# Optimization experiments

Measured on AMD Instinct MI355X. Metric: run time of the kernel, lower is better.

The kernel has to match this reference:

```python
import jax, jax.numpy as jnp
import numpy as np

B, N, F_IN, DIM, TOPK = 64, 1024, 10, 64, 20
EPS = 1e-5  # BatchNorm eps
NEG_SLOPE = 0.2


def _bn_eval(x, gamma, beta, mean, var):
    # eval-mode BatchNorm1d over the channel (last) axis
    return (x - mean) * jax.lax.rsqrt(var + EPS) * gamma + beta


def setup_inputs() -> dict:
    key = jax.random.key(0)
    ks = jax.random.split(key, 10)
    return {
        "data": jax.random.normal(ks[0], (B, N, F_IN), jnp.float32),
        "emb": jax.random.normal(ks[1], (N, DIM), jnp.float32),
        "W_lin": jax.random.normal(ks[2], (F_IN, DIM), jnp.float32),
        "att_i": jax.random.normal(ks[3], (DIM,), jnp.float32),
        "att_j": jax.random.normal(ks[4], (DIM,), jnp.float32),
        "att_em_i": jax.random.normal(ks[5], (DIM,), jnp.float32),
        "att_em_j": jax.random.normal(ks[6], (DIM,), jnp.float32),
        "gnn_bias": jax.random.normal(ks[7], (DIM,), jnp.float32),
        "bn1_gamma": jnp.ones((DIM,), jnp.float32),
        "bn1_beta": jnp.zeros((DIM,), jnp.float32),
        "bn1_mean": jnp.zeros((DIM,), jnp.float32),
        "bn1_var": jnp.ones((DIM,), jnp.float32),
        "bn2_gamma": jnp.ones((DIM,), jnp.float32),
        "bn2_beta": jnp.zeros((DIM,), jnp.float32),
        "bn2_mean": jnp.zeros((DIM,), jnp.float32),
        "bn2_var": jnp.ones((DIM,), jnp.float32),
        "out_W": jax.random.normal(ks[8], (DIM, 1), jnp.float32),
        "out_b": jax.random.normal(ks[9], (1,), jnp.float32),
    }


def reference(data, emb, W_lin, att_i, att_j, att_em_i, att_em_j, gnn_bias,
              bn1_gamma, bn1_beta, bn1_mean, bn1_var,
              bn2_gamma, bn2_beta, bn2_mean, bn2_var, out_W, out_b):
    Bn, Nn, _ = data.shape
    BN_nodes = Bn * Nn
    x = data.reshape(BN_nodes, -1)                      # [B*N, F_IN] (input is detached in torch)

    # ---- dynamic graph: cosine similarity of (detached) node embeddings, top-k per row ----
    w = jax.lax.stop_gradient(emb)                      # weights_arr = embedding.detach()
    norms = jnp.linalg.norm(w, axis=-1)                 # [N]
    cos = (w @ w.T) / (norms[:, None] * norms[None, :])  # [N, N]
    topk_idx = jax.lax.top_k(cos, TOPK)[1]              # [N, K], gated_j (message sources)
    src = topk_idx.reshape(-1)                          # j
    dst = jnp.repeat(jnp.arange(Nn), TOPK)              # i
    offs = (jnp.arange(Bn) * Nn)[:, None]               # per-graph node offsets
    bsrc = (src[None, :] + offs).reshape(-1)            # [B*N*K]
    bdst = (dst[None, :] + offs).reshape(-1)
    self_mask = bsrc == bdst                            # edges killed by remove_self_loops
    loops = jnp.arange(BN_nodes)                        # add_self_loops
    e_src = jnp.concatenate([bsrc, loops])              # [E]
    e_dst = jnp.concatenate([bdst, loops])
    e_mask = jnp.concatenate([self_mask, jnp.zeros(BN_nodes, bool)])

    # ---- GAT-style attention message passing (heads=1, concat=False, aggr='add') ----
    h = x @ W_lin                                       # [B*N, DIM]
    h_i, h_j = h[e_dst], h[e_src]                       # gathers, [E, DIM]
    emb_i = emb[e_dst % Nn]                             # embedding repeated per batch graph
    emb_j = emb[e_src % Nn]
    logit = (h_i * att_i).sum(-1) + (emb_i * att_em_i).sum(-1) \
          + (h_j * att_j).sum(-1) + (emb_j * att_em_j).sum(-1)  # [E]
    logit = jnp.where(logit > 0, logit, NEG_SLOPE * logit)       # leaky_relu(0.2)
    logit = jnp.where(e_mask, -1e30, logit)             # removed self-loops get zero weight
    seg_max = jax.ops.segment_max(logit, e_dst, num_segments=BN_nodes)
    ex = jnp.where(e_mask, 0.0, jnp.exp(logit - seg_max[e_dst]))
    seg_sum = jax.ops.segment_sum(ex, e_dst, num_segments=BN_nodes)
    alpha = ex / seg_sum[e_dst]                         # segment softmax over incoming edges
    agg = jax.ops.segment_sum(h_j * alpha[:, None], e_dst, num_segments=BN_nodes)
    agg = agg + gnn_bias                                # [B*N, DIM]
    gcn = jax.nn.relu(_bn_eval(agg, bn1_gamma, bn1_beta, bn1_mean, bn1_var))

    # ---- output head: multiply by node embedding, BN+ReLU, Linear(DIM->1) ----
    y = gcn.reshape(Bn, Nn, DIM) * emb[None, :, :]
    y = jax.nn.relu(_bn_eval(y, bn2_gamma, bn2_beta, bn2_mean, bn2_var))
    out = y @ out_W + out_b                             # [B, N, 1]; dropout is inference no-op
    return out.reshape(Bn, Nn)
```

## Files before the change

kernel.cpp:

```cpp
#include <hip/hip_runtime.h>
#include <hip/hip_bf16.h>

#define N_NODES 1024
#define B_SZ 64
#define F_IN 10
#define DIM 64
#define TOPK 20
#define BN_TOT (B_SZ * N_NODES)

#define GT_BLKS 256
#define HS_BLKS 4096
#define AB_BLKS (GT_BLKS + 1 + HS_BLKS)

__global__ __launch_bounds__(256) void k_build(
    const float* __restrict__ data, const float* __restrict__ emb,
    const float* __restrict__ W_lin,
    const float* __restrict__ att_i, const float* __restrict__ att_j,
    const float* __restrict__ att_em_i, const float* __restrict__ att_em_j,
    const float* __restrict__ gnn_bias,
    const float* __restrict__ g1, const float* __restrict__ b1,
    const float* __restrict__ m1, const float* __restrict__ v1,
    const float* __restrict__ g2, const float* __restrict__ b2,
    const float* __restrict__ m2, const float* __restrict__ v2,
    __hip_bfloat16* __restrict__ h, float* __restrict__ ddt,
    float* __restrict__ sst, int* __restrict__ tk, float4* __restrict__ bnp) {
    const int bid = blockIdx.x;
    const int t = threadIdx.x;
    const int lane = t & 63, w = t >> 6;

    if (bid < GT_BLKS) {
        __shared__ float As[4][64];
        __shared__ float P[64][65];
        const int r0 = bid * 4;
        As[t >> 6][t & 63] = emb[(r0 + (t >> 6)) * DIM + (t & 63)];
        __syncthreads();
        float av = As[w][lane];
        float nni = av * av;
#pragma unroll
        for (int m = 32; m >= 1; m >>= 1) nni += __shfl_xor(nni, m, 64);
        const float ni = sqrtf(nni);
        float v[16];
        for (int p = 0; p < 16; ++p) {
            __syncthreads();
#pragma unroll
            for (int k = 0; k < 16; ++k) {
                int idx = t + k * 256;
                P[idx >> 6][idx & 63] = emb[(p * 64 + (idx >> 6)) * DIM + (idx & 63)];
            }
            __syncthreads();
            float dot = 0.f, nsq = 0.f;
#pragma unroll
            for (int d = 0; d < 64; ++d) {
                float pv = P[lane][d];
                dot = fmaf(As[w][d], pv, dot);
                nsq = fmaf(pv, pv, nsq);
            }
            v[p] = dot / (ni * sqrtf(nsq));
        }
        int* tkr = tk + (r0 + w) * TOPK;
        for (int it = 0; it < TOPK; ++it) {
            float bv = v[0];
            int bp = 0;
#pragma unroll
            for (int p = 1; p < 16; ++p)
                if (v[p] > bv) { bv = v[p]; bp = p; }
            int bidx = lane + bp * 64;
#pragma unroll
            for (int m = 32; m >= 1; m >>= 1) {
                float ov = __shfl_xor(bv, m, 64);
                int oi = __shfl_xor(bidx, m, 64);
                if (ov > bv || (ov == bv && oi < bidx)) { bv = ov; bidx = oi; }
            }
            if (lane == 0) tkr[it] = bidx;
            if ((bidx & 63) == lane) v[bidx >> 6] = -3.0e38f;
        }
        return;
    }

    if (bid == GT_BLKS) {
        if (t < DIM) {
            float a1 = g1[t] * rsqrtf(v1[t] + 1e-5f);
            float c1 = (gnn_bias[t] - m1[t]) * a1 + b1[t];
            float a2 = g2[t] * rsqrtf(v2[t] + 1e-5f);
            float c2 = b2[t] - m2[t] * a2;
            bnp[t] = make_float4(a1, c1, a2, c2);
        }
        return;
    }

    {
        const int base = (bid - GT_BLKS - 1) * 16 + w * 4;
        float wl[F_IN];
#pragma unroll
        for (int f = 0; f < F_IN; ++f) wl[f] = W_lin[f * DIM + lane];
        const float ai = att_i[lane], aj = att_j[lane];
        const float aei = att_em_i[lane], aej = att_em_j[lane];
#pragma unroll
        for (int r = 0; r < 4; ++r) {
            const int node = base + r;
            const int i = node & (N_NODES - 1);
            const float ev = emb[i * DIM + lane];
            const float* dp = data + node * F_IN;
            float hv = 0.f;
#pragma unroll
            for (int f = 0; f < F_IN; ++f) hv = fmaf(dp[f], wl[f], hv);
            h[node * DIM + lane] = __float2bfloat16(hv);
            float s1 = fmaf(hv, ai, ev * aei);
            float s2 = fmaf(hv, aj, ev * aej);
#pragma unroll
            for (int m = 32; m >= 1; m >>= 1) {
                s1 += __shfl_xor(s1, m, 64);
                s2 += __shfl_xor(s2, m, 64);
            }
            if (lane == 0) { ddt[node] = s1; sst[node] = s2; }
        }
    }
}

__global__ __launch_bounds__(256) void k_main(
    const __hip_bfloat16* __restrict__ h, const float* __restrict__ emb,
    const float* __restrict__ ddt, const float* __restrict__ sst,
    const int* __restrict__ tk, const float4* __restrict__ bnp,
    const float* __restrict__ outW, const float* __restrict__ outB,
    float* __restrict__ out) {
    const int bid = blockIdx.x;
    const int nb = (bid & 7) * 2048 + (bid >> 3);
    const int w = threadIdx.x >> 6, lane = threadIdx.x & 63;
    const int node = nb * 4 + w;
    const int i = node & (N_NODES - 1);
    const int bbase = node & ~(N_NODES - 1);

    int j = i;
    if (lane < TOPK) j = tk[i * TOPK + lane];

    float sv = 0.f;
    if (lane <= TOPK) sv = sst[bbase + j];
    const float ddv = ddt[node];

    const __hip_bfloat16* hb = h + (size_t)bbase * DIM + lane;
    float hvf[TOPK + 1];
#pragma unroll
    for (int k = 0; k < TOPK; ++k) {
        int jk = __builtin_amdgcn_readlane(j, k);
        hvf[k] = __bfloat162float(hb[(size_t)jk * DIM]);
    }
    hvf[TOPK] = __bfloat162float(hb[(size_t)i * DIM]);

    const bool masked = (lane < TOPK) && (j == i);
    float lg = -3.0e38f;
    if (lane <= TOPK) {
        float l = ddv + sv;
        l = (l > 0.f) ? l : 0.2f * l;
        lg = masked ? -3.0e38f : l;
    }
    float m = lg;
#pragma unroll
    for (int mm = 16; mm >= 1; mm >>= 1) m = fmaxf(m, __shfl_xor(m, mm, 64));
    float ex = (lane <= TOPK && !masked) ? __expf(lg - m) : 0.f;
    float s = ex;
#pragma unroll
    for (int mm = 16; mm >= 1; mm >>= 1) s += __shfl_xor(s, mm, 64);
    const float alpha = ex / s;

    float agg = 0.f;
#pragma unroll
    for (int k = 0; k <= TOPK; ++k) {
        int ab = __builtin_amdgcn_readlane(__float_as_int(alpha), k);
        agg = fmaf(__int_as_float(ab), hvf[k], agg);
    }

    const float4 p = bnp[lane];
    float x1 = fmaxf(fmaf(agg, p.x, p.y), 0.f);
    float y = x1 * emb[i * DIM + lane];
    float x2 = fmaxf(fmaf(y, p.z, p.w), 0.f);
    float o = x2 * outW[lane];
#pragma unroll
    for (int mm = 32; mm >= 1; mm >>= 1) o += __shfl_xor(o, mm, 64);
    if (lane == 0) out[node] = o + outB[0];
}

extern "C" void kernel_launch(void* const* d_in, const int* in_sizes, int n_in,
                              void* d_out, int out_size, void* d_ws, size_t ws_size,
                              hipStream_t stream) {
    const float* data     = (const float*)d_in[0];
    const float* emb      = (const float*)d_in[1];
    const float* W_lin    = (const float*)d_in[2];
    const float* att_i    = (const float*)d_in[3];
    const float* att_j    = (const float*)d_in[4];
    const float* att_em_i = (const float*)d_in[5];
    const float* att_em_j = (const float*)d_in[6];
    const float* gnn_bias = (const float*)d_in[7];
    const float* g1 = (const float*)d_in[8];
    const float* b1 = (const float*)d_in[9];
    const float* m1 = (const float*)d_in[10];
    const float* v1 = (const float*)d_in[11];
    const float* g2 = (const float*)d_in[12];
    const float* b2 = (const float*)d_in[13];
    const float* m2 = (const float*)d_in[14];
    const float* v2 = (const float*)d_in[15];
    const float* outW = (const float*)d_in[16];
    const float* outB = (const float*)d_in[17];
    float* out = (float*)d_out;

    char* ws = (char*)d_ws;
    __hip_bfloat16* h = (__hip_bfloat16*)ws;
    float* ddt  = (float*)(ws + (size_t)8 * 1024 * 1024);
    float* sst  = ddt + BN_TOT;
    int*   tk   = (int*)(sst + BN_TOT);
    float4* bnp = (float4*)(tk + N_NODES * TOPK);

    k_build<<<AB_BLKS, 256, 0, stream>>>(
        data, emb, W_lin, att_i, att_j, att_em_i, att_em_j, gnn_bias,
        g1, b1, m1, v1, g2, b2, m2, v2,
        h, ddt, sst, tk, bnp);
    k_main<<<BN_TOT / 4, 256, 0, stream>>>(h, emb, ddt, sst, tk, bnp,
                                           outW, outB, out);
}
```

Measured before the change: 68.01 us.

## Split cosine top-k into separate kernel with transposed embeddings and precomputed norms

The cosine-similarity top-k moves out of the build kernel into its own kernel with one 128-thread block per row. A pre-pass transposes the embedding matrix and computes reciprocal norms, so each thread computes 8 contiguous dot products with coalesced float4 loads. Each wave selects its own top-20 and one wave merges the two candidate lists. This spreads the work over 1024 blocks instead of 256 serial-heavy blocks, at the cost of an extra kernel launch, extra workspace, and a dependency between launches.

```diff
diff --git a/kernel.cpp b/kernel.cpp
--- a/kernel.cpp
+++ b/kernel.cpp
@@ -8,11 +8,12 @@
 #define TOPK 20
 #define BN_TOT (B_SZ * N_NODES)
 
-#define GT_BLKS 256
+#define TR_BLKS 16
+#define PREP_BLKS 256
 #define HS_BLKS 4096
-#define AB_BLKS (GT_BLKS + 1 + HS_BLKS)
-
-__global__ __launch_bounds__(256) void k_build(
+#define K0_BLKS (TR_BLKS + PREP_BLKS + 1 + HS_BLKS)
+
+__global__ __launch_bounds__(256) void k_pre(
     const float* __restrict__ data, const float* __restrict__ emb,
     const float* __restrict__ W_lin,
     const float* __restrict__ att_i, const float* __restrict__ att_j,
@@ -22,62 +23,42 @@
     const float* __restrict__ m1, const float* __restrict__ v1,
     const float* __restrict__ g2, const float* __restrict__ b2,
     const float* __restrict__ m2, const float* __restrict__ v2,
+    float* __restrict__ embT, float* __restrict__ rn,
     __hip_bfloat16* __restrict__ h, float* __restrict__ ddt,
-    float* __restrict__ sst, int* __restrict__ tk, float4* __restrict__ bnp) {
+    float* __restrict__ sst, float4* __restrict__ bnp) {
     const int bid = blockIdx.x;
     const int t = threadIdx.x;
     const int lane = t & 63, w = t >> 6;
 
-    if (bid < GT_BLKS) {
-        __shared__ float As[4][64];
-        __shared__ float P[64][65];
-        const int r0 = bid * 4;
-        As[t >> 6][t & 63] = emb[(r0 + (t >> 6)) * DIM + (t & 63)];
+    if (bid < TR_BLKS) {
+        __shared__ float T[64][65];
+        const int r0 = bid * 64;
+#pragma unroll
+        for (int k = 0; k < 16; ++k) {
+            int idx = t + k * 256;
+            T[idx >> 6][idx & 63] = emb[(r0 + (idx >> 6)) * DIM + (idx & 63)];
+        }
         __syncthreads();
-        float av = As[w][lane];
-        float nni = av * av;
-#pragma unroll
-        for (int m = 32; m >= 1; m >>= 1) nni += __shfl_xor(nni, m, 64);
-        const float ni = sqrtf(nni);
-        float v[16];
-        for (int p = 0; p < 16; ++p) {
-            __syncthreads();
-#pragma unroll
-            for (int k = 0; k < 16; ++k) {
-                int idx = t + k * 256;
-                P[idx >> 6][idx & 63] = emb[(p * 64 + (idx >> 6)) * DIM + (idx & 63)];
-            }
-            __syncthreads();
-            float dot = 0.f, nsq = 0.f;
-#pragma unroll
-            for (int d = 0; d < 64; ++d) {
-                float pv = P[lane][d];
-                dot = fmaf(As[w][d], pv, dot);
-                nsq = fmaf(pv, pv, nsq);
-            }
-            v[p] = dot / (ni * sqrtf(nsq));
-        }
-        int* tkr = tk + (r0 + w) * TOPK;
-        for (int it = 0; it < TOPK; ++it) {
-            float bv = v[0];
-            int bp = 0;
-#pragma unroll
-            for (int p = 1; p < 16; ++p)
-                if (v[p] > bv) { bv = v[p]; bp = p; }
-            int bidx = lane + bp * 64;
-#pragma unroll
-            for (int m = 32; m >= 1; m >>= 1) {
-                float ov = __shfl_xor(bv, m, 64);
-                int oi = __shfl_xor(bidx, m, 64);
-                if (ov > bv || (ov == bv && oi < bidx)) { bv = ov; bidx = oi; }
-            }
-            if (lane == 0) tkr[it] = bidx;
-            if ((bidx & 63) == lane) v[bidx >> 6] = -3.0e38f;
+#pragma unroll
+        for (int k = 0; k < 16; ++k) {
+            int idx = t + k * 256;
+            int d = idx >> 6, j = idx & 63;
+            embT[d * N_NODES + r0 + j] = T[j][d];
         }
         return;
     }
 
-    if (bid == GT_BLKS) {
+    if (bid < TR_BLKS + PREP_BLKS) {
+        const int node = (bid - TR_BLKS) * 4 + w;
+        float e = emb[node * DIM + lane];
+        float t3 = e * e;
+#pragma unroll
+        for (int m = 32; m >= 1; m >>= 1) t3 += __shfl_xor(t3, m, 64);
+        if (lane == 0) rn[node] = rsqrtf(t3);
+        return;
+    }
+
+    if (bid == TR_BLKS + PREP_BLKS) {
         if (t < DIM) {
             float a1 = g1[t] * rsqrtf(v1[t] + 1e-5f);
             float c1 = (gnn_bias[t] - m1[t]) * a1 + b1[t];
@@ -89,7 +70,7 @@
     }
 
     {
-        const int base = (bid - GT_BLKS - 1) * 16 + w * 4;
+        const int base = (bid - TR_BLKS - PREP_BLKS - 1) * 16 + w * 4;
         float wl[F_IN];
 #pragma unroll
         for (int f = 0; f < F_IN; ++f) wl[f] = W_lin[f * DIM + lane];
@@ -113,6 +94,83 @@
                 s2 += __shfl_xor(s2, m, 64);
             }
             if (lane == 0) { ddt[node] = s1; sst[node] = s2; }
+        }
+    }
+}
+
+__global__ __launch_bounds__(128) void k_gt(
+    const float* __restrict__ emb, const float* __restrict__ embT,
+    const float* __restrict__ rn, int* __restrict__ tk) {
+    __shared__ float cv[2][20];
+    __shared__ int ci[2][20];
+    const int row = blockIdx.x;
+    const int w = threadIdx.x >> 6, lane = threadIdx.x & 63;
+    const int c0 = w * 512 + lane * 8;
+
+    const float rni = rn[row];
+    const float4 rc0 = *(const float4*)(rn + c0);
+    const float4 rc1 = *(const float4*)(rn + c0 + 4);
+
+    const float* __restrict__ ar = emb + row * DIM;
+    float dot[8] = {};
+#pragma unroll
+    for (int d = 0; d < 64; ++d) {
+        const float ad = ar[d];
+        const float* tr = embT + d * N_NODES + c0;
+        const float4 p0 = *(const float4*)tr;
+        const float4 p1 = *(const float4*)(tr + 4);
+        dot[0] = fmaf(ad, p0.x, dot[0]);
+        dot[1] = fmaf(ad, p0.y, dot[1]);
+        dot[2] = fmaf(ad, p0.z, dot[2]);
+        dot[3] = fmaf(ad, p0.w, dot[3]);
+        dot[4] = fmaf(ad, p1.x, dot[4]);
+        dot[5] = fmaf(ad, p1.y, dot[5]);
+        dot[6] = fmaf(ad, p1.z, dot[6]);
+        dot[7] = fmaf(ad, p1.w, dot[7]);
+    }
+    float v[8];
+    v[0] = dot[0] * rni * rc0.x;
+    v[1] = dot[1] * rni * rc0.y;
+    v[2] = dot[2] * rni * rc0.z;
+    v[3] = dot[3] * rni * rc0.w;
+    v[4] = dot[4] * rni * rc1.x;
+    v[5] = dot[5] * rni * rc1.y;
+    v[6] = dot[6] * rni * rc1.z;
+    v[7] = dot[7] * rni * rc1.w;
+
+    for (int it = 0; it < TOPK; ++it) {
+        float bv = v[0];
+        int bq = 0;
+#pragma unroll
+        for (int q = 1; q < 8; ++q)
+            if (v[q] > bv) { bv = v[q]; bq = q; }
+        int bidx = c0 + bq;
+#pragma unroll
+        for (int m = 32; m >= 1; m >>= 1) {
+            float ov = __shfl_xor(bv, m, 64);
+            int oi = __shfl_xor(bidx, m, 64);
+            if (ov > bv || (ov == bv && oi < bidx)) { bv = ov; bidx = oi; }
+        }
+        if (lane == 0) { cv[w][it] = bv; ci[w][it] = bidx; }
+        if (((bidx >> 3) & 63) == lane && (bidx >> 9) == w) v[bidx & 7] = -3.0e38f;
+    }
+    __syncthreads();
+
+    if (w == 0) {
+        float mval = -3.0e38f;
+        int midx = 0x7fffffff;
+        if (lane < 2 * TOPK) { mval = cv[lane / 20][lane % 20]; midx = ci[lane / 20][lane % 20]; }
+        for (int it = 0; it < TOPK; ++it) {
+            float bv = mval;
+            int bidx = midx;
+#pragma unroll
+            for (int m = 32; m >= 1; m >>= 1) {
+                float ov = __shfl_xor(bv, m, 64);
+                int oi = __shfl_xor(bidx, m, 64);
+                if (ov > bv || (ov == bv && oi < bidx)) { bv = ov; bidx = oi; }
+            }
+            if (lane == 0) tk[row * TOPK + it] = bidx;
+            if (midx == bidx) mval = -3.0e38f;
         }
     }
 }
@@ -204,15 +262,18 @@
 
     char* ws = (char*)d_ws;
     __hip_bfloat16* h = (__hip_bfloat16*)ws;
-    float* ddt  = (float*)(ws + (size_t)8 * 1024 * 1024);
+    float* embT = (float*)(ws + ((size_t)8 << 20));
+    float* ddt  = embT + (size_t)DIM * N_NODES;
     float* sst  = ddt + BN_TOT;
-    int*   tk   = (int*)(sst + BN_TOT);
+    float* rn   = sst + BN_TOT;
+    int*   tk   = (int*)(rn + N_NODES);
     float4* bnp = (float4*)(tk + N_NODES * TOPK);
 
-    k_build<<<AB_BLKS, 256, 0, stream>>>(
+    k_pre<<<K0_BLKS, 256, 0, stream>>>(
         data, emb, W_lin, att_i, att_j, att_em_i, att_em_j, gnn_bias,
         g1, b1, m1, v1, g2, b2, m2, v2,
-        h, ddt, sst, tk, bnp);
+        embT, rn, h, ddt, sst, bnp);
+    k_gt<<<N_NODES, 128, 0, stream>>>(emb, embT, rn, tk);
     k_main<<<BN_TOT / 4, 256, 0, stream>>>(h, emb, ddt, sst, tk, bnp,
                                            outW, outB, out);
 }
```

Result: slower. 84.50 us (+24.3%).

## Compute cosine top-k with one block per row and two-stage merge

Applied to the files above, without the earlier changes.

The similarity/top-k stage changes from one block per 4 rows, which looped over shared-memory tiles, to one block per row. Each thread computes 4 candidate columns directly from global memory with float4 loads. Each wavefront picks a local top-20, and a final wave merges the 80 candidates through LDS. The goal is more parallelism and less serialized shared-memory tiling in the graph-building stage. The trade-off is redundant global reads of the embedding matrix for every row, plus an extra merge step and launch bounds hint.

```diff
diff --git a/kernel.cpp b/kernel.cpp
--- a/kernel.cpp
+++ b/kernel.cpp
@@ -8,11 +8,11 @@
 #define TOPK 20
 #define BN_TOT (B_SZ * N_NODES)
 
-#define GT_BLKS 256
+#define GT_BLKS 1024
 #define HS_BLKS 4096
-#define AB_BLKS (GT_BLKS + 1 + HS_BLKS)
-
-__global__ __launch_bounds__(256) void k_build(
+#define K1_BLKS (GT_BLKS + HS_BLKS + 1)
+
+__global__ __launch_bounds__(256, 2) void k_build(
     const float* __restrict__ data, const float* __restrict__ emb,
     const float* __restrict__ W_lin,
     const float* __restrict__ att_i, const float* __restrict__ att_j,
@@ -29,67 +29,96 @@
     const int lane = t & 63, w = t >> 6;
 
     if (bid < GT_BLKS) {
-        __shared__ float As[4][64];
-        __shared__ float P[64][65];
-        const int r0 = bid * 4;
-        As[t >> 6][t & 63] = emb[(r0 + (t >> 6)) * DIM + (t & 63)];
-        __syncthreads();
-        float av = As[w][lane];
-        float nni = av * av;
-#pragma unroll
-        for (int m = 32; m >= 1; m >>= 1) nni += __shfl_xor(nni, m, 64);
-        const float ni = sqrtf(nni);
-        float v[16];
-        for (int p = 0; p < 16; ++p) {
-            __syncthreads();
-#pragma unroll
-            for (int k = 0; k < 16; ++k) {
-                int idx = t + k * 256;
-                P[idx >> 6][idx & 63] = emb[(p * 64 + (idx >> 6)) * DIM + (idx & 63)];
-            }
-            __syncthreads();
-            float dot = 0.f, nsq = 0.f;
-#pragma unroll
-            for (int d = 0; d < 64; ++d) {
-                float pv = P[lane][d];
-                dot = fmaf(As[w][d], pv, dot);
-                nsq = fmaf(pv, pv, nsq);
-            }
-            v[p] = dot / (ni * sqrtf(nsq));
-        }
-        int* tkr = tk + (r0 + w) * TOPK;
+        __shared__ float cv[4 * TOPK];
+        __shared__ int ci[4 * TOPK];
+        const int row = bid;
+        const int j0 = t * 4;
+        const float* __restrict__ ar = emb + row * DIM;
+
+        float asq = 0.f;
+#pragma unroll
+        for (int d = 0; d < 64; ++d) asq = fmaf(ar[d], ar[d], asq);
+        const float rni = rsqrtf(asq);
+
+        float dt[4] = {0.f, 0.f, 0.f, 0.f};
+        float ns[4] = {0.f, 0.f, 0.f, 0.f};
+#pragma unroll
+        for (int lq = 0; lq < 4; ++lq) {
+            const int d0 = lq * 16;
+            float4 P[4][4];
+#pragma unroll
+            for (int r = 0; r < 4; ++r)
+#pragma unroll
+                for (int q = 0; q < 4; ++q)
+                    P[r][q] = *(const float4*)(emb + (j0 + r) * DIM + d0 + q * 4);
+            float a[16];
+#pragma unroll
+            for (int d = 0; d < 16; ++d) a[d] = ar[d0 + d];
+#pragma unroll
+            for (int r = 0; r < 4; ++r) {
+#pragma unroll
+                for (int q = 0; q < 4; ++q) {
+                    dt[r] = fmaf(a[q * 4 + 0], P[r][q].x, dt[r]);
+                    ns[r] = fmaf(P[r][q].x, P[r][q].x, ns[r]);
+                    dt[r] = fmaf(a[q * 4 + 1], P[r][q].y, dt[r]);
+                    ns[r] = fmaf(P[r][q].y, P[r][q].y, ns[r]);
+                    dt[r] = fmaf(a[q * 4 + 2], P[r][q].z, dt[r]);
+                    ns[r] = fmaf(P[r][q].z, P[r][q].z, ns[r]);
+                    dt[r] = fmaf(a[q * 4 + 3], P[r][q].w, dt[r]);
+                    ns[r] = fmaf(P[r][q].w, P[r][q].w, ns[r]);
+                }
+            }
+        }
+        float v0 = dt[0] * rni * rsqrtf(ns[0]);
+        float v1 = dt[1] * rni * rsqrtf(ns[1]);
+        float v2 = dt[2] * rni * rsqrtf(ns[2]);
+        float v3 = dt[3] * rni * rsqrtf(ns[3]);
+
         for (int it = 0; it < TOPK; ++it) {
-            float bv = v[0];
-            int bp = 0;
-#pragma unroll
-            for (int p = 1; p < 16; ++p)
-                if (v[p] > bv) { bv = v[p]; bp = p; }
-            int bidx = lane + bp * 64;
+            float bv = v0; int bq = 0;
+            if (v1 > bv) { bv = v1; bq = 1; }
+            if (v2 > bv) { bv = v2; bq = 2; }
+            if (v3 > bv) { bv = v3; bq = 3; }
+            int bidx = j0 + bq;
 #pragma unroll
             for (int m = 32; m >= 1; m >>= 1) {
                 float ov = __shfl_xor(bv, m, 64);
                 int oi = __shfl_xor(bidx, m, 64);
                 if (ov > bv || (ov == bv && oi < bidx)) { bv = ov; bidx = oi; }
             }
-            if (lane == 0) tkr[it] = bidx;
-            if ((bidx & 63) == lane) v[bidx >> 6] = -3.0e38f;
+            if (lane == 0) { cv[w * TOPK + it] = bv; ci[w * TOPK + it] = bidx; }
+            v0 = (j0 + 0 == bidx) ? -3.0e38f : v0;
+            v1 = (j0 + 1 == bidx) ? -3.0e38f : v1;
+            v2 = (j0 + 2 == bidx) ? -3.0e38f : v2;
+            v3 = (j0 + 3 == bidx) ? -3.0e38f : v3;
+        }
+        __syncthreads();
+
+        if (w == 0) {
+            float m0 = cv[lane];
+            int i0 = ci[lane];
+            float m1 = -3.0e38f;
+            int i1 = 0x7fffffff;
+            if (lane < 16) { m1 = cv[64 + lane]; i1 = ci[64 + lane]; }
+            for (int it = 0; it < TOPK; ++it) {
+                float bv = m0; int bidx = i0;
+                if (m1 > bv || (m1 == bv && i1 < bidx)) { bv = m1; bidx = i1; }
+#pragma unroll
+                for (int m = 32; m >= 1; m >>= 1) {
+                    float ov = __shfl_xor(bv, m, 64);
+                    int oi = __shfl_xor(bidx, m, 64);
+                    if (ov > bv || (ov == bv && oi < bidx)) { bv = ov; bidx = oi; }
+                }
+                if (lane == 0) tk[row * TOPK + it] = bidx;
+                if (i0 == bidx) m0 = -3.0e38f;
+                if (i1 == bidx) m1 = -3.0e38f;
+            }
         }
         return;
     }
 
-    if (bid == GT_BLKS) {
-        if (t < DIM) {
-            float a1 = g1[t] * rsqrtf(v1[t] + 1e-5f);
-            float c1 = (gnn_bias[t] - m1[t]) * a1 + b1[t];
-            float a2 = g2[t] * rsqrtf(v2[t] + 1e-5f);
-            float c2 = b2[t] - m2[t] * a2;
-            bnp[t] = make_float4(a1, c1, a2, c2);
-        }
-        return;
-    }
-
-    {
-        const int base = (bid - GT_BLKS - 1) * 16 + w * 4;
+    if (bid < GT_BLKS + HS_BLKS) {
+        const int base = (bid - GT_BLKS) * 16 + w * 4;
         float wl[F_IN];
 #pragma unroll
         for (int f = 0; f < F_IN; ++f) wl[f] = W_lin[f * DIM + lane];
@@ -114,6 +143,15 @@
             }
             if (lane == 0) { ddt[node] = s1; sst[node] = s2; }
         }
+        return;
+    }
+
+    if (t < DIM) {
+        float a1 = g1[t] * rsqrtf(v1[t] + 1e-5f);
+        float c1 = (gnn_bias[t] - m1[t]) * a1 + b1[t];
+        float a2 = g2[t] * rsqrtf(v2[t] + 1e-5f);
+        float c2 = b2[t] - m2[t] * a2;
+        bnp[t] = make_float4(a1, c1, a2, c2);
     }
 }
 
@@ -204,12 +242,12 @@
 
     char* ws = (char*)d_ws;
     __hip_bfloat16* h = (__hip_bfloat16*)ws;
-    float* ddt  = (float*)(ws + (size_t)8 * 1024 * 1024);
+    float* ddt  = (float*)(ws + ((size_t)8 << 20));
     float* sst  = ddt + BN_TOT;
     int*   tk   = (int*)(sst + BN_TOT);
     float4* bnp = (float4*)(tk + N_NODES * TOPK);
 
-    k_build<<<AB_BLKS, 256, 0, stream>>>(
+    k_build<<<K1_BLKS, 256, 0, stream>>>(
         data, emb, W_lin, att_i, att_j, att_em_i, att_em_j, gnn_bias,
         g1, b1, m1, v1, g2, b2, m2, v2,
         h, ddt, sst, tk, bnp);
```

Result: slower. 110.2 us (+62.1%).
